# Kernel optimization log

Measured on AMD Instinct MI355X. Metric: run time of the kernel, lower is better.

Reference implementation:

```python
import jax, jax.numpy as jnp
import numpy as np
import math

B, H, T, N = 2, 16, 4096, 64  # N = mlp_internal_dim_multiplier * n_embd // n_head = 1*1024//16
THETA = 2.0 ** 16


def _cos_sin(T, N):
    # quantized-theta RoPE tables, matching get_freqs + angle construction
    t = jnp.arange(N, dtype=jnp.float32)
    tq = jnp.floor(t / 2.0) * 2.0                      # quantize(t, q=2)
    freqs = 1.0 / (THETA ** (tq / N)) / (2.0 * math.pi)  # [N]
    phases = jnp.arange(T, dtype=jnp.float32)[:, None] * freqs[None, :]  # [T,N]
    ang = (phases % 1.0) * (2.0 * math.pi)
    return jnp.cos(ang), jnp.sin(ang)                  # each [T,N]


def setup_inputs() -> dict:
    key = jax.random.key(0)
    kq, kv = jax.random.split(key)
    Q = jax.random.normal(kq, (B, H, T, N), dtype=jnp.float32)
    V = jax.random.normal(kv, (B, H, T, N), dtype=jnp.float32)
    return {"Q": Q, "V": V}


def reference(Q, V):
    # K is Q (asserted in the torch module); RoPE applied to Q only.
    b, h, t, n = Q.shape
    cos, sin = _cos_sin(t, n)                          # [t,n], broadcast over b,h
    q_rot = jnp.stack((-Q[..., 1::2], Q[..., ::2]), axis=-1).reshape(Q.shape)
    QR = Q * cos + q_rot * sin                         # [b,h,t,n]
    scores = jnp.einsum('bhtn,bhsn->bhts', QR, QR) * (n ** -0.5)
    # strict lower-triangular mask (tril with diagonal=-1): no softmax
    mask = jnp.tril(jnp.ones((t, t), dtype=bool), k=-1)
    scores = jnp.where(mask, scores, 0.0)
    return jnp.einsum('bhts,bhsn->bhtn', scores, V)
```

## Files before the change

kernel.cpp:

```cpp
#include <hip/hip_runtime.h>

#define T_SEQ 4096
#define NDIM 64
#define BH 32
#define TN (T_SEQ * NDIM)

typedef short short8 __attribute__((ext_vector_type(8)));
typedef float f32x16 __attribute__((ext_vector_type(16)));
typedef unsigned uint2e __attribute__((ext_vector_type(2)));

static __device__ __forceinline__ unsigned packbf(float lo, float hi) {
    unsigned r;
    asm("v_cvt_pk_bf16_f32 %0, %1, %2" : "=v"(r) : "v"(lo), "v"(hi));
    return r;
}
static __device__ __forceinline__ f32x16 mfma32(short8 a, short8 b, f32x16 c) {
    return __builtin_amdgcn_mfma_f32_32x32x16_bf16(a, b, c, 0, 0, 0);
}

static __device__ __forceinline__ void half_swap(unsigned &x, unsigned &y) {
#if __has_builtin(__builtin_amdgcn_permlane32_swap)
    uint2e r = __builtin_amdgcn_permlane32_swap(x, y, false, false);
    x = r[0]; y = r[1];
#else
    int sl = (((int)threadIdx.x & 63) ^ 32) << 2;
    unsigned bx = (unsigned)__builtin_amdgcn_ds_bpermute(sl, (int)x);
    unsigned by = (unsigned)__builtin_amdgcn_ds_bpermute(sl, (int)y);
    bool hi = (threadIdx.x & 32) != 0;
    unsigned nx = hi ? by : x;
    unsigned ny = hi ? y : bx;
    x = nx; y = ny;
#endif
}

static __device__ __forceinline__ void tile_to_frags(const f32x16 &sc, short8 &f0, short8 &f1) {
    unsigned d[4][2];
#pragma unroll
    for (int g = 0; g < 4; ++g) {
        d[g][0] = packbf(sc[4 * g + 0], sc[4 * g + 1]);
        d[g][1] = packbf(sc[4 * g + 2], sc[4 * g + 3]);
    }
    half_swap(d[0][0], d[1][0]);
    half_swap(d[0][1], d[1][1]);
    half_swap(d[2][0], d[3][0]);
    half_swap(d[2][1], d[3][1]);
    union { unsigned u[4]; short8 s; } a, b;
    a.u[0] = d[0][0]; a.u[1] = d[0][1]; a.u[2] = d[1][0]; a.u[3] = d[1][1];
    b.u[0] = d[2][0]; b.u[1] = d[2][1]; b.u[2] = d[3][0]; b.u[3] = d[3][1];
    f0 = a.s; f1 = b.s;
}

__global__ __launch_bounds__(256) void prep_kernel(const float* __restrict__ Q,
                                                   const float* __restrict__ V,
                                                   unsigned short* __restrict__ qf,
                                                   unsigned short* __restrict__ vfr) {
    __shared__ float tile[128 * 65];
    const int bx = blockIdx.x;
    const int tid = threadIdx.x;
    if (bx < 1024) {
        const int bh = bx >> 5;
        const int rb = bx & 31;
        const int tl = tid >> 3;
        const int hijw = tid & 7;
        const float fbase = exp2f(-0.5f * (float)hijw) * 0.15915494309189535f;
        const float2* qsrc = (const float2*)(Q + ((size_t)bh * T_SEQ + rb * 128) * NDIM);
        unsigned* qdst = (unsigned*)(qf + (size_t)bh * TN) + rb * 4096;
        const float kmul[4] = {1.0f, 0.0625f, 0.00390625f, 2.44140625e-4f};
#pragma unroll 4
        for (int it = 0; it < 16; ++it) {
            const int kc = it & 3;
            const int tb4 = it >> 2;
            const int row = tb4 * 32 + tl;
            const int t = rb * 128 + row;
            const int np = kc * 8 + hijw;
            float2 q = qsrc[row * 32 + np];
            const float freq = fbase * kmul[kc];
            float ph = (float)t * freq;
            float ang = (ph - floorf(ph)) * 6.283185307179586f;
            float s, c;
            __sincosf(ang, &s, &c);
            float r0 = q.x * c - q.y * s;
            float r1 = q.y * c + q.x * s;
            qdst[it * 256 + tid] = packbf(r0, r1);
        }
    } else {
        const int b2 = bx - 1024;
        const int sb = b2 & 31;
        const int bh = b2 >> 5;
        const float* vsrc = V + ((size_t)bh * T_SEQ + sb * 128) * NDIM;
#pragma unroll
        for (int i = 0; i < 8; ++i) {
            int e = (i * 256 + tid) * 4;
            int row = e >> 6, col = e & 63;
            float4 d4 = *(const float4*)(vsrc + e);
            tile[row * 65 + col + 0] = d4.x; tile[row * 65 + col + 1] = d4.y;
            tile[row * 65 + col + 2] = d4.z; tile[row * 65 + col + 3] = d4.w;
        }
        __syncthreads();
        unsigned short* dst = vfr + (size_t)bh * TN + (size_t)sb * 8192;
#pragma unroll
        for (int u = 0; u < 4; ++u) {
            int g = u * 256 + tid;
            int kc = g >> 7, dh = g & 127;
            int d = dh >> 1, hh = dh & 1;
            int sbase = kc * 16 + hh * 8;
            uint4 o;
            o.x = packbf(tile[(sbase + 0) * 65 + d] * 0.125f, tile[(sbase + 1) * 65 + d] * 0.125f);
            o.y = packbf(tile[(sbase + 2) * 65 + d] * 0.125f, tile[(sbase + 3) * 65 + d] * 0.125f);
            o.z = packbf(tile[(sbase + 4) * 65 + d] * 0.125f, tile[(sbase + 5) * 65 + d] * 0.125f);
            o.w = packbf(tile[(sbase + 6) * 65 + d] * 0.125f, tile[(sbase + 7) * 65 + d] * 0.125f);
            *(uint4*)(dst + g * 8) = o;
        }
    }
}

static __device__ __forceinline__ void load_ak4(const unsigned short* qfh, int sb, int ws,
                                                int lhx16, short8 (&A)[2][4]) {
    const int r32base = sb * 4 + 2 * ws;
#pragma unroll
    for (int st2 = 0; st2 < 2; ++st2)
#pragma unroll
        for (int kc = 0; kc < 4; ++kc)
            A[st2][kc] = *(const short8*)(qfh + (size_t)((r32base + st2) * 4 + kc) * 512 + lhx16);
}
static __device__ __forceinline__ void load_vf8(const unsigned short* vfh, int sb, int ws,
                                                int lhx16, short8 (&V)[4][2]) {
#pragma unroll
    for (int kc4 = 0; kc4 < 4; ++kc4) {
        const size_t base = (size_t)sb * 8192 + (size_t)(4 * ws + kc4) * 1024 + lhx16;
        V[kc4][0] = *(const short8*)(vfh + base);
        V[kc4][1] = *(const short8*)(vfh + base + 512);
    }
}
static __device__ __forceinline__ void s_phase(const short8 (&ak)[2][4], const short8 (&bq)[2][4],
                                               const f32x16 &zc, f32x16 (&sacc)[2][2]) {
#pragma unroll
    for (int st2 = 0; st2 < 2; ++st2)
#pragma unroll
        for (int tt2 = 0; tt2 < 2; ++tt2) {
            f32x16 acc = mfma32(ak[st2][0], bq[tt2][0], zc);
            acc = mfma32(ak[st2][1], bq[tt2][1], acc);
            acc = mfma32(ak[st2][2], bq[tt2][2], acc);
            sacc[st2][tt2] = mfma32(ak[st2][3], bq[tt2][3], acc);
        }
}
static __device__ __forceinline__ void transform_all(const f32x16 (&sacc)[2][2], short8 (&pa)[2][4]) {
#pragma unroll
    for (int st2 = 0; st2 < 2; ++st2)
#pragma unroll
        for (int tt2 = 0; tt2 < 2; ++tt2)
            tile_to_frags(sacc[st2][tt2], pa[tt2][2 * st2 + 0], pa[tt2][2 * st2 + 1]);
}
static __device__ __forceinline__ void o_phase(const short8 (&pa)[2][4], const short8 (&vf)[4][2],
                                               f32x16 (&oacc)[2][2]) {
#pragma unroll
    for (int kc4 = 0; kc4 < 4; ++kc4) {
        oacc[0][0] = mfma32(pa[0][kc4], vf[kc4][0], oacc[0][0]);
        oacc[0][1] = mfma32(pa[0][kc4], vf[kc4][1], oacc[0][1]);
        oacc[1][0] = mfma32(pa[1][kc4], vf[kc4][0], oacc[1][0]);
        oacc[1][1] = mfma32(pa[1][kc4], vf[kc4][1], oacc[1][1]);
    }
}

__global__ __launch_bounds__(256, 2) void attn_kernel(const unsigned short* __restrict__ qf,
                                                      const unsigned short* __restrict__ vfr,
                                                      float* __restrict__ out) {
    __shared__ float4 red[2][4][4][64];

    const int tid = threadIdx.x;
    const int lane = tid & 63;
    const int w = tid >> 6;
    const int ws = w >> 1, wt = w & 1;
    const int l31 = lane & 31, hi = lane >> 5;

    const int blk = blockIdx.x;
    const int bh = blk & 31;
    const int qb = 31 - (blk >> 5);
    const int t0 = qb * 128;

    const unsigned short* qfh = qf + (size_t)bh * TN;
    const unsigned short* vfh = vfr + (size_t)bh * TN;
    float* out_h = out + (size_t)bh * TN;

    const int lhx16 = (l31 * 2 + hi) * 8;

    short8 bq[2][4];
#pragma unroll
    for (int tt2 = 0; tt2 < 2; ++tt2) {
        const int r32 = (t0 >> 5) + 2 * wt + tt2;
#pragma unroll
        for (int kc = 0; kc < 4; ++kc)
            bq[tt2][kc] = *(const short8*)(qfh + (size_t)(r32 * 4 + kc) * 512 + lhx16);
    }

    f32x16 zc;
#pragma unroll
    for (int r = 0; r < 16; ++r) zc[r] = 0.0f;

    f32x16 oacc[2][2];
#pragma unroll
    for (int a = 0; a < 2; ++a)
#pragma unroll
        for (int b = 0; b < 2; ++b)
#pragma unroll
            for (int r = 0; r < 16; ++r) oacc[a][b][r] = 0.0f;

    short8 ak[2][4], vf[4][2];
    f32x16 sacc[2][2];
    load_ak4(qfh, 0, ws, lhx16, ak);
    load_vf8(vfh, 0, ws, lhx16, vf);
    s_phase(ak, bq, zc, sacc);
    load_ak4(qfh, (1 <= qb ? 1 : qb), ws, lhx16, ak);

    for (int sb = 0; sb < qb; ++sb) {
        short8 pa[2][4];
        transform_all(sacc, pa);
        o_phase(pa, vf, oacc);
        load_vf8(vfh, sb + 1, ws, lhx16, vf);
        s_phase(ak, bq, zc, sacc);
        const int nak = (sb + 2 <= qb) ? sb + 2 : qb;
        load_ak4(qfh, nak, ws, lhx16, ak);
    }

    {
#pragma unroll
        for (int st2 = 0; st2 < 2; ++st2) {
            const int st = 2 * ws + st2;
#pragma unroll
            for (int tt2 = 0; tt2 < 2; ++tt2) {
                const int tg = (2 * wt + tt2) * 32 + l31;
#pragma unroll
                for (int r = 0; r < 16; ++r) {
                    const int sg = st * 32 + (r & 3) + 8 * (r >> 2) + 4 * hi;
                    if (sg >= tg) sacc[st2][tt2][r] = 0.0f;
                }
            }
        }
        short8 pa[2][4];
        transform_all(sacc, pa);
        o_phase(pa, vf, oacc);
    }

    if (ws == 1) {
#pragma unroll
        for (int tt2 = 0; tt2 < 2; ++tt2)
#pragma unroll
            for (int dd = 0; dd < 2; ++dd)
#pragma unroll
                for (int g = 0; g < 4; ++g) {
                    float4 v;
                    v.x = oacc[tt2][dd][4 * g + 0];
                    v.y = oacc[tt2][dd][4 * g + 1];
                    v.z = oacc[tt2][dd][4 * g + 2];
                    v.w = oacc[tt2][dd][4 * g + 3];
                    red[wt][tt2 * 2 + dd][g][lane] = v;
                }
    }
    __syncthreads();
    if (ws == 0) {
#pragma unroll
        for (int tt2 = 0; tt2 < 2; ++tt2)
#pragma unroll
            for (int dd = 0; dd < 2; ++dd) {
#pragma unroll
                for (int g = 0; g < 4; ++g) {
                    float4 o = red[wt][tt2 * 2 + dd][g][lane];
                    oacc[tt2][dd][4 * g + 0] += o.x;
                    oacc[tt2][dd][4 * g + 1] += o.y;
                    oacc[tt2][dd][4 * g + 2] += o.z;
                    oacc[tt2][dd][4 * g + 3] += o.w;
                }
#pragma unroll
                for (int r = 0; r < 16; ++r) {
                    const int rl = (r & 3) + 8 * (r >> 2) + 4 * hi;
                    out_h[(size_t)(t0 + 64 * wt + 32 * tt2 + rl) * NDIM + 32 * dd + l31] =
                        oacc[tt2][dd][r];
                }
            }
    }
}

extern "C" void kernel_launch(void* const* d_in, const int* in_sizes, int n_in,
                              void* d_out, int out_size, void* d_ws, size_t ws_size,
                              hipStream_t stream) {
    (void)in_sizes; (void)n_in; (void)out_size; (void)ws_size;
    const float* Q = (const float*)d_in[0];
    const float* V = (const float*)d_in[1];
    float* out = (float*)d_out;

    unsigned short* qf  = (unsigned short*)d_ws;
    unsigned short* vfr = qf + (size_t)BH * TN;

    prep_kernel<<<2048, 256, 0, stream>>>(Q, V, qf, vfr);
    attn_kernel<<<BH * 32, 256, 0, stream>>>(qf, vfr, out);
}
```

Baseline: 167.8 us.

## Fuse prep and attention into one persistent kernel with per-head dataflow flags

Merges the RoPE/V-transpose prep kernel and the attention kernel into a single launch. Blocks take work items from an atomic ticket counter: the first 2048 tickets do prep tasks and bump a per-head completion counter, and later tickets run attention for a head once its counter reaches 64. This is meant to remove the kernel boundary and let attention on ready heads overlap prep for other heads. In exchange it adds a memset, atomic traffic and spin-waiting. Every block also carries the larger shared-memory footprint, which may lower occupancy.

Measured after the change: 320.2 us. 90.9% more time.

```diff
diff --git a/kernel.cpp b/kernel.cpp
--- a/kernel.cpp
+++ b/kernel.cpp
@@ -50,6 +50,269 @@
     f0 = a.s; f1 = b.s;
 }
 
+
+static __device__ __forceinline__ void rope_task(const float* __restrict__ Q,
+                                                 unsigned short* __restrict__ qf,
+                                                 int bh, int rb, int tid) {
+    const int tl = tid >> 3;
+    const int hijw = tid & 7;
+    const float fbase = exp2f(-0.5f * (float)hijw) * 0.15915494309189535f;
+    const float2* qsrc = (const float2*)(Q + ((size_t)bh * T_SEQ + rb * 128) * NDIM);
+    unsigned* qdst = (unsigned*)(qf + (size_t)bh * TN) + rb * 4096;
+    const float kmul[4] = {1.0f, 0.0625f, 0.00390625f, 2.44140625e-4f};
+#pragma unroll 4
+    for (int it = 0; it < 16; ++it) {
+        const int kc = it & 3;
+        const int row = (it >> 2) * 32 + tl;
+        const int t = rb * 128 + row;
+        const int np = kc * 8 + hijw;
+        float2 q = qsrc[row * 32 + np];
+        const float freq = fbase * kmul[kc];
+        float ph = (float)t * freq;
+        float ang = (ph - floorf(ph)) * 6.283185307179586f;
+        float s, c;
+        __sincosf(ang, &s, &c);
+        float r0 = q.x * c - q.y * s;
+        float r1 = q.y * c + q.x * s;
+        qdst[it * 256 + tid] = packbf(r0, r1);
+    }
+}
+
+static __device__ __forceinline__ void vtrans_task(const float* __restrict__ V,
+                                                   unsigned short* __restrict__ vfr,
+                                                   int bh, int sb, int tid, float* tile) {
+    const float* vsrc = V + ((size_t)bh * T_SEQ + sb * 128) * NDIM;
+#pragma unroll
+    for (int i = 0; i < 8; ++i) {
+        int e = (i * 256 + tid) * 4;
+        int row = e >> 6, col = e & 63;
+        float4 d4 = *(const float4*)(vsrc + e);
+        tile[row * 65 + col + 0] = d4.x; tile[row * 65 + col + 1] = d4.y;
+        tile[row * 65 + col + 2] = d4.z; tile[row * 65 + col + 3] = d4.w;
+    }
+    __syncthreads();
+    unsigned short* dst = vfr + (size_t)bh * TN + (size_t)sb * 8192;
+#pragma unroll
+    for (int u = 0; u < 4; ++u) {
+        int g = u * 256 + tid;
+        int kc = g >> 7, dh = g & 127;
+        int d = dh >> 1, hh = dh & 1;
+        int sbase = kc * 16 + hh * 8;
+        uint4 o;
+        o.x = packbf(tile[(sbase + 0) * 65 + d] * 0.125f, tile[(sbase + 1) * 65 + d] * 0.125f);
+        o.y = packbf(tile[(sbase + 2) * 65 + d] * 0.125f, tile[(sbase + 3) * 65 + d] * 0.125f);
+        o.z = packbf(tile[(sbase + 4) * 65 + d] * 0.125f, tile[(sbase + 5) * 65 + d] * 0.125f);
+        o.w = packbf(tile[(sbase + 6) * 65 + d] * 0.125f, tile[(sbase + 7) * 65 + d] * 0.125f);
+        *(uint4*)(dst + g * 8) = o;
+    }
+}
+
+static __device__ __forceinline__ void load_ak4(const unsigned short* qfh, int sb, int ws,
+                                                int lhx16, short8 (&A)[2][4]) {
+    const int r32base = sb * 4 + 2 * ws;
+#pragma unroll
+    for (int st2 = 0; st2 < 2; ++st2)
+#pragma unroll
+        for (int kc = 0; kc < 4; ++kc)
+            A[st2][kc] = *(const short8*)(qfh + (size_t)((r32base + st2) * 4 + kc) * 512 + lhx16);
+}
+static __device__ __forceinline__ void load_vf8(const unsigned short* vfh, int sb, int ws,
+                                                int lhx16, short8 (&V)[4][2]) {
+#pragma unroll
+    for (int kc4 = 0; kc4 < 4; ++kc4) {
+        const size_t base = (size_t)sb * 8192 + (size_t)(4 * ws + kc4) * 1024 + lhx16;
+        V[kc4][0] = *(const short8*)(vfh + base);
+        V[kc4][1] = *(const short8*)(vfh + base + 512);
+    }
+}
+static __device__ __forceinline__ void s_phase(const short8 (&ak)[2][4], const short8 (&bq)[2][4],
+                                               const f32x16 &zc, f32x16 (&sacc)[2][2]) {
+#pragma unroll
+    for (int st2 = 0; st2 < 2; ++st2)
+#pragma unroll
+        for (int tt2 = 0; tt2 < 2; ++tt2) {
+            f32x16 acc = mfma32(ak[st2][0], bq[tt2][0], zc);
+            acc = mfma32(ak[st2][1], bq[tt2][1], acc);
+            acc = mfma32(ak[st2][2], bq[tt2][2], acc);
+            sacc[st2][tt2] = mfma32(ak[st2][3], bq[tt2][3], acc);
+        }
+}
+static __device__ __forceinline__ void transform_all(const f32x16 (&sacc)[2][2], short8 (&pa)[2][4]) {
+#pragma unroll
+    for (int st2 = 0; st2 < 2; ++st2)
+#pragma unroll
+        for (int tt2 = 0; tt2 < 2; ++tt2)
+            tile_to_frags(sacc[st2][tt2], pa[tt2][2 * st2 + 0], pa[tt2][2 * st2 + 1]);
+}
+static __device__ __forceinline__ void o_phase(const short8 (&pa)[2][4], const short8 (&vf)[4][2],
+                                               f32x16 (&oacc)[2][2]) {
+#pragma unroll
+    for (int kc4 = 0; kc4 < 4; ++kc4) {
+        oacc[0][0] = mfma32(pa[0][kc4], vf[kc4][0], oacc[0][0]);
+        oacc[0][1] = mfma32(pa[0][kc4], vf[kc4][1], oacc[0][1]);
+        oacc[1][0] = mfma32(pa[1][kc4], vf[kc4][0], oacc[1][0]);
+        oacc[1][1] = mfma32(pa[1][kc4], vf[kc4][1], oacc[1][1]);
+    }
+}
+
+static __device__ __forceinline__ void attn_block_body(const unsigned short* __restrict__ qf,
+                                                       const unsigned short* __restrict__ vfr,
+                                                       float* __restrict__ out,
+                                                       int bh, int qb, int tid, char* smem) {
+    const int lane = tid & 63;
+    const int w = tid >> 6;
+    const int ws = w >> 1, wt = w & 1;
+    const int l31 = lane & 31, hi = lane >> 5;
+    const int t0 = qb * 128;
+
+    const unsigned short* qfh = qf + (size_t)bh * TN;
+    const unsigned short* vfh = vfr + (size_t)bh * TN;
+    float* out_h = out + (size_t)bh * TN;
+
+    const int lhx16 = (l31 * 2 + hi) * 8;
+
+    short8 bq[2][4];
+#pragma unroll
+    for (int tt2 = 0; tt2 < 2; ++tt2) {
+        const int r32 = (t0 >> 5) + 2 * wt + tt2;
+#pragma unroll
+        for (int kc = 0; kc < 4; ++kc)
+            bq[tt2][kc] = *(const short8*)(qfh + (size_t)(r32 * 4 + kc) * 512 + lhx16);
+    }
+
+    f32x16 zc;
+#pragma unroll
+    for (int r = 0; r < 16; ++r) zc[r] = 0.0f;
+
+    f32x16 oacc[2][2];
+#pragma unroll
+    for (int a = 0; a < 2; ++a)
+#pragma unroll
+        for (int b = 0; b < 2; ++b)
+#pragma unroll
+            for (int r = 0; r < 16; ++r) oacc[a][b][r] = 0.0f;
+
+    short8 ak[2][4], vf[4][2];
+    f32x16 sacc[2][2];
+    load_ak4(qfh, 0, ws, lhx16, ak);
+    load_vf8(vfh, 0, ws, lhx16, vf);
+    s_phase(ak, bq, zc, sacc);
+    load_ak4(qfh, (1 <= qb ? 1 : qb), ws, lhx16, ak);
+
+    for (int sb = 0; sb < qb; ++sb) {
+        short8 pa[2][4];
+        transform_all(sacc, pa);
+        o_phase(pa, vf, oacc);
+        load_vf8(vfh, sb + 1, ws, lhx16, vf);
+        s_phase(ak, bq, zc, sacc);
+        const int nak = (sb + 2 <= qb) ? sb + 2 : qb;
+        load_ak4(qfh, nak, ws, lhx16, ak);
+    }
+
+    {
+#pragma unroll
+        for (int st2 = 0; st2 < 2; ++st2) {
+            const int st = 2 * ws + st2;
+#pragma unroll
+            for (int tt2 = 0; tt2 < 2; ++tt2) {
+                const int tg = (2 * wt + tt2) * 32 + l31;
+#pragma unroll
+                for (int r = 0; r < 16; ++r) {
+                    const int sg = st * 32 + (r & 3) + 8 * (r >> 2) + 4 * hi;
+                    if (sg >= tg) sacc[st2][tt2][r] = 0.0f;
+                }
+            }
+        }
+        short8 pa[2][4];
+        transform_all(sacc, pa);
+        o_phase(pa, vf, oacc);
+    }
+
+    float4* redp = (float4*)smem;
+    if (ws == 1) {
+#pragma unroll
+        for (int tt2 = 0; tt2 < 2; ++tt2)
+#pragma unroll
+            for (int dd = 0; dd < 2; ++dd)
+#pragma unroll
+                for (int g = 0; g < 4; ++g) {
+                    float4 v;
+                    v.x = oacc[tt2][dd][4 * g + 0];
+                    v.y = oacc[tt2][dd][4 * g + 1];
+                    v.z = oacc[tt2][dd][4 * g + 2];
+                    v.w = oacc[tt2][dd][4 * g + 3];
+                    redp[((wt * 4 + (tt2 * 2 + dd)) * 4 + g) * 64 + lane] = v;
+                }
+    }
+    __syncthreads();
+    if (ws == 0) {
+#pragma unroll
+        for (int tt2 = 0; tt2 < 2; ++tt2)
+#pragma unroll
+            for (int dd = 0; dd < 2; ++dd) {
+#pragma unroll
+                for (int g = 0; g < 4; ++g) {
+                    float4 o = redp[((wt * 4 + (tt2 * 2 + dd)) * 4 + g) * 64 + lane];
+                    oacc[tt2][dd][4 * g + 0] += o.x;
+                    oacc[tt2][dd][4 * g + 1] += o.y;
+                    oacc[tt2][dd][4 * g + 2] += o.z;
+                    oacc[tt2][dd][4 * g + 3] += o.w;
+                }
+#pragma unroll
+                for (int r = 0; r < 16; ++r) {
+                    const int rl = (r & 3) + 8 * (r >> 2) + 4 * hi;
+                    out_h[(size_t)(t0 + 64 * wt + 32 * tt2 + rl) * NDIM + 32 * dd + l31] =
+                        oacc[tt2][dd][r];
+                }
+            }
+    }
+}
+
+__global__ __launch_bounds__(256, 2) void fused_kernel(const float* __restrict__ Q,
+                                                       const float* __restrict__ V,
+                                                       unsigned short* __restrict__ qf,
+                                                       unsigned short* __restrict__ vfr,
+                                                       float* __restrict__ out,
+                                                       unsigned* __restrict__ ctrl) {
+    __shared__ __align__(16) char smem_all[33280];
+    __shared__ unsigned sh_task;
+
+    const int tid = threadIdx.x;
+    if (tid == 0)
+        sh_task = __hip_atomic_fetch_add(&ctrl[0], 1u, __ATOMIC_RELAXED,
+                                         __HIP_MEMORY_SCOPE_AGENT);
+    __syncthreads();
+    const unsigned task = sh_task;
+
+    if (task < 2048u) {
+        const int bh = (int)(task & 31u);
+        if (task < 1024u) {
+            rope_task(Q, qf, bh, (int)(task >> 5), tid);
+        } else {
+            vtrans_task(V, vfr, bh, (int)((task - 1024u) >> 5), tid, (float*)smem_all);
+        }
+        __syncthreads();
+        if (tid == 0) {
+            __builtin_amdgcn_fence(__ATOMIC_RELEASE, "agent");
+            __hip_atomic_fetch_add(&ctrl[16 + bh], 1u, __ATOMIC_RELAXED,
+                                   __HIP_MEMORY_SCOPE_AGENT);
+        }
+    } else {
+        const unsigned t = task - 2048u;
+        const int bh = (int)(t & 31u);
+        const int qb = 31 - (int)(t >> 5);
+        if (tid == 0) {
+            while (__hip_atomic_load(&ctrl[16 + bh], __ATOMIC_RELAXED,
+                                     __HIP_MEMORY_SCOPE_AGENT) < 64u)
+                __builtin_amdgcn_s_sleep(16);
+            __builtin_amdgcn_fence(__ATOMIC_ACQUIRE, "agent");
+        }
+        __syncthreads();
+        __builtin_amdgcn_fence(__ATOMIC_ACQUIRE, "agent");
+        attn_block_body(qf, vfr, out, bh, qb, tid, smem_all);
+    }
+}
+
 __global__ __launch_bounds__(256) void prep_kernel(const float* __restrict__ Q,
                                                    const float* __restrict__ V,
                                                    unsigned short* __restrict__ qf,
@@ -58,239 +321,38 @@
     const int bx = blockIdx.x;
     const int tid = threadIdx.x;
     if (bx < 1024) {
-        const int bh = bx >> 5;
-        const int rb = bx & 31;
-        const int tl = tid >> 3;
-        const int hijw = tid & 7;
-        const float fbase = exp2f(-0.5f * (float)hijw) * 0.15915494309189535f;
-        const float2* qsrc = (const float2*)(Q + ((size_t)bh * T_SEQ + rb * 128) * NDIM);
-        unsigned* qdst = (unsigned*)(qf + (size_t)bh * TN) + rb * 4096;
-        const float kmul[4] = {1.0f, 0.0625f, 0.00390625f, 2.44140625e-4f};
-#pragma unroll 4
-        for (int it = 0; it < 16; ++it) {
-            const int kc = it & 3;
-            const int tb4 = it >> 2;
-            const int row = tb4 * 32 + tl;
-            const int t = rb * 128 + row;
-            const int np = kc * 8 + hijw;
-            float2 q = qsrc[row * 32 + np];
-            const float freq = fbase * kmul[kc];
-            float ph = (float)t * freq;
-            float ang = (ph - floorf(ph)) * 6.283185307179586f;
-            float s, c;
-            __sincosf(ang, &s, &c);
-            float r0 = q.x * c - q.y * s;
-            float r1 = q.y * c + q.x * s;
-            qdst[it * 256 + tid] = packbf(r0, r1);
-        }
+        rope_task(Q, qf, bx >> 5, bx & 31, tid);
     } else {
         const int b2 = bx - 1024;
-        const int sb = b2 & 31;
-        const int bh = b2 >> 5;
-        const float* vsrc = V + ((size_t)bh * T_SEQ + sb * 128) * NDIM;
-#pragma unroll
-        for (int i = 0; i < 8; ++i) {
-            int e = (i * 256 + tid) * 4;
-            int row = e >> 6, col = e & 63;
-            float4 d4 = *(const float4*)(vsrc + e);
-            tile[row * 65 + col + 0] = d4.x; tile[row * 65 + col + 1] = d4.y;
-            tile[row * 65 + col + 2] = d4.z; tile[row * 65 + col + 3] = d4.w;
-        }
-        __syncthreads();
-        unsigned short* dst = vfr + (size_t)bh * TN + (size_t)sb * 8192;
-#pragma unroll
-        for (int u = 0; u < 4; ++u) {
-            int g = u * 256 + tid;
-            int kc = g >> 7, dh = g & 127;
-            int d = dh >> 1, hh = dh & 1;
-            int sbase = kc * 16 + hh * 8;
-            uint4 o;
-            o.x = packbf(tile[(sbase + 0) * 65 + d] * 0.125f, tile[(sbase + 1) * 65 + d] * 0.125f);
-            o.y = packbf(tile[(sbase + 2) * 65 + d] * 0.125f, tile[(sbase + 3) * 65 + d] * 0.125f);
-            o.z = packbf(tile[(sbase + 4) * 65 + d] * 0.125f, tile[(sbase + 5) * 65 + d] * 0.125f);
-            o.w = packbf(tile[(sbase + 6) * 65 + d] * 0.125f, tile[(sbase + 7) * 65 + d] * 0.125f);
-            *(uint4*)(dst + g * 8) = o;
-        }
-    }
-}
-
-static __device__ __forceinline__ void load_ak4(const unsigned short* qfh, int sb, int ws,
-                                                int lhx16, short8 (&A)[2][4]) {
-    const int r32base = sb * 4 + 2 * ws;
-#pragma unroll
-    for (int st2 = 0; st2 < 2; ++st2)
-#pragma unroll
-        for (int kc = 0; kc < 4; ++kc)
-            A[st2][kc] = *(const short8*)(qfh + (size_t)((r32base + st2) * 4 + kc) * 512 + lhx16);
-}
-static __device__ __forceinline__ void load_vf8(const unsigned short* vfh, int sb, int ws,
-                                                int lhx16, short8 (&V)[4][2]) {
-#pragma unroll
-    for (int kc4 = 0; kc4 < 4; ++kc4) {
-        const size_t base = (size_t)sb * 8192 + (size_t)(4 * ws + kc4) * 1024 + lhx16;
-        V[kc4][0] = *(const short8*)(vfh + base);
-        V[kc4][1] = *(const short8*)(vfh + base + 512);
-    }
-}
-static __device__ __forceinline__ void s_phase(const short8 (&ak)[2][4], const short8 (&bq)[2][4],
-                                               const f32x16 &zc, f32x16 (&sacc)[2][2]) {
-#pragma unroll
-    for (int st2 = 0; st2 < 2; ++st2)
-#pragma unroll
-        for (int tt2 = 0; tt2 < 2; ++tt2) {
-            f32x16 acc = mfma32(ak[st2][0], bq[tt2][0], zc);
-            acc = mfma32(ak[st2][1], bq[tt2][1], acc);
-            acc = mfma32(ak[st2][2], bq[tt2][2], acc);
-            sacc[st2][tt2] = mfma32(ak[st2][3], bq[tt2][3], acc);
-        }
-}
-static __device__ __forceinline__ void transform_all(const f32x16 (&sacc)[2][2], short8 (&pa)[2][4]) {
-#pragma unroll
-    for (int st2 = 0; st2 < 2; ++st2)
-#pragma unroll
-        for (int tt2 = 0; tt2 < 2; ++tt2)
-            tile_to_frags(sacc[st2][tt2], pa[tt2][2 * st2 + 0], pa[tt2][2 * st2 + 1]);
-}
-static __device__ __forceinline__ void o_phase(const short8 (&pa)[2][4], const short8 (&vf)[4][2],
-                                               f32x16 (&oacc)[2][2]) {
-#pragma unroll
-    for (int kc4 = 0; kc4 < 4; ++kc4) {
-        oacc[0][0] = mfma32(pa[0][kc4], vf[kc4][0], oacc[0][0]);
-        oacc[0][1] = mfma32(pa[0][kc4], vf[kc4][1], oacc[0][1]);
-        oacc[1][0] = mfma32(pa[1][kc4], vf[kc4][0], oacc[1][0]);
-        oacc[1][1] = mfma32(pa[1][kc4], vf[kc4][1], oacc[1][1]);
-    }
-}
-
+        vtrans_task(V, vfr, b2 >> 5, b2 & 31, tid, tile);
+    }
+}
 __global__ __launch_bounds__(256, 2) void attn_kernel(const unsigned short* __restrict__ qf,
                                                       const unsigned short* __restrict__ vfr,
                                                       float* __restrict__ out) {
-    __shared__ float4 red[2][4][4][64];
-
-    const int tid = threadIdx.x;
-    const int lane = tid & 63;
-    const int w = tid >> 6;
-    const int ws = w >> 1, wt = w & 1;
-    const int l31 = lane & 31, hi = lane >> 5;
-
+    __shared__ __align__(16) char red[32768];
     const int blk = blockIdx.x;
-    const int bh = blk & 31;
-    const int qb = 31 - (blk >> 5);
-    const int t0 = qb * 128;
-
-    const unsigned short* qfh = qf + (size_t)bh * TN;
-    const unsigned short* vfh = vfr + (size_t)bh * TN;
-    float* out_h = out + (size_t)bh * TN;
-
-    const int lhx16 = (l31 * 2 + hi) * 8;
-
-    short8 bq[2][4];
-#pragma unroll
-    for (int tt2 = 0; tt2 < 2; ++tt2) {
-        const int r32 = (t0 >> 5) + 2 * wt + tt2;
-#pragma unroll
-        for (int kc = 0; kc < 4; ++kc)
-            bq[tt2][kc] = *(const short8*)(qfh + (size_t)(r32 * 4 + kc) * 512 + lhx16);
-    }
-
-    f32x16 zc;
-#pragma unroll
-    for (int r = 0; r < 16; ++r) zc[r] = 0.0f;
-
-    f32x16 oacc[2][2];
-#pragma unroll
-    for (int a = 0; a < 2; ++a)
-#pragma unroll
-        for (int b = 0; b < 2; ++b)
-#pragma unroll
-            for (int r = 0; r < 16; ++r) oacc[a][b][r] = 0.0f;
-
-    short8 ak[2][4], vf[4][2];
-    f32x16 sacc[2][2];
-    load_ak4(qfh, 0, ws, lhx16, ak);
-    load_vf8(vfh, 0, ws, lhx16, vf);
-    s_phase(ak, bq, zc, sacc);
-    load_ak4(qfh, (1 <= qb ? 1 : qb), ws, lhx16, ak);
-
-    for (int sb = 0; sb < qb; ++sb) {
-        short8 pa[2][4];
-        transform_all(sacc, pa);
-        o_phase(pa, vf, oacc);
-        load_vf8(vfh, sb + 1, ws, lhx16, vf);
-        s_phase(ak, bq, zc, sacc);
-        const int nak = (sb + 2 <= qb) ? sb + 2 : qb;
-        load_ak4(qfh, nak, ws, lhx16, ak);
-    }
-
-    {
-#pragma unroll
-        for (int st2 = 0; st2 < 2; ++st2) {
-            const int st = 2 * ws + st2;
-#pragma unroll
-            for (int tt2 = 0; tt2 < 2; ++tt2) {
-                const int tg = (2 * wt + tt2) * 32 + l31;
-#pragma unroll
-                for (int r = 0; r < 16; ++r) {
-                    const int sg = st * 32 + (r & 3) + 8 * (r >> 2) + 4 * hi;
-                    if (sg >= tg) sacc[st2][tt2][r] = 0.0f;
-                }
-            }
-        }
-        short8 pa[2][4];
-        transform_all(sacc, pa);
-        o_phase(pa, vf, oacc);
-    }
-
-    if (ws == 1) {
-#pragma unroll
-        for (int tt2 = 0; tt2 < 2; ++tt2)
-#pragma unroll
-            for (int dd = 0; dd < 2; ++dd)
-#pragma unroll
-                for (int g = 0; g < 4; ++g) {
-                    float4 v;
-                    v.x = oacc[tt2][dd][4 * g + 0];
-                    v.y = oacc[tt2][dd][4 * g + 1];
-                    v.z = oacc[tt2][dd][4 * g + 2];
-                    v.w = oacc[tt2][dd][4 * g + 3];
-                    red[wt][tt2 * 2 + dd][g][lane] = v;
-                }
-    }
-    __syncthreads();
-    if (ws == 0) {
-#pragma unroll
-        for (int tt2 = 0; tt2 < 2; ++tt2)
-#pragma unroll
-            for (int dd = 0; dd < 2; ++dd) {
-#pragma unroll
-                for (int g = 0; g < 4; ++g) {
-                    float4 o = red[wt][tt2 * 2 + dd][g][lane];
-                    oacc[tt2][dd][4 * g + 0] += o.x;
-                    oacc[tt2][dd][4 * g + 1] += o.y;
-                    oacc[tt2][dd][4 * g + 2] += o.z;
-                    oacc[tt2][dd][4 * g + 3] += o.w;
-                }
-#pragma unroll
-                for (int r = 0; r < 16; ++r) {
-                    const int rl = (r & 3) + 8 * (r >> 2) + 4 * hi;
-                    out_h[(size_t)(t0 + 64 * wt + 32 * tt2 + rl) * NDIM + 32 * dd + l31] =
-                        oacc[tt2][dd][r];
-                }
-            }
-    }
+    attn_block_body(qf, vfr, out, blk & 31, 31 - (blk >> 5), threadIdx.x, red);
 }
 
 extern "C" void kernel_launch(void* const* d_in, const int* in_sizes, int n_in,
                               void* d_out, int out_size, void* d_ws, size_t ws_size,
                               hipStream_t stream) {
-    (void)in_sizes; (void)n_in; (void)out_size; (void)ws_size;
+    (void)in_sizes; (void)n_in; (void)out_size;
     const float* Q = (const float*)d_in[0];
     const float* V = (const float*)d_in[1];
     float* out = (float*)d_out;
 
     unsigned short* qf  = (unsigned short*)d_ws;
     unsigned short* vfr = qf + (size_t)BH * TN;
-
-    prep_kernel<<<2048, 256, 0, stream>>>(Q, V, qf, vfr);
-    attn_kernel<<<BH * 32, 256, 0, stream>>>(qf, vfr, out);
-}
+    const size_t data_bytes = (size_t)2 * BH * TN * sizeof(unsigned short);
+
+    if (ws_size >= data_bytes + 256) {
+        unsigned* ctrl = (unsigned*)((char*)d_ws + data_bytes);
+        (void)hipMemsetAsync(ctrl, 0, 256, stream);
+        fused_kernel<<<3072, 256, 0, stream>>>(Q, V, qf, vfr, out, ctrl);
+    } else {
+        prep_kernel<<<2048, 256, 0, stream>>>(Q, V, qf, vfr);
+        attn_kernel<<<BH * 32, 256, 0, stream>>>(qf, vfr, out);
+    }
+}
```
